# Optimization experiments

Hardware: AMD Instinct MI355X
Metric: run time of the kernel (lower is better)

## Reference

```python
import jax, jax.numpy as jnp
import numpy as np

EPS = 1e-10
WS = 5  # window_size
PAD = WS // 2


def _conv(x, k, pad_h, pad_w):
    # x: [N,1,H,W], k: [1,1,kh,kw], 'same'-style explicit padding
    return jax.lax.conv_general_dilated(
        x, k, window_strides=(1, 1),
        padding=[(pad_h, pad_h), (pad_w, pad_w)],
        dimension_numbers=("NCHW", "OIHW", "NCHW"))


def setup_inputs() -> dict:
    key = jax.random.key(0)
    B, C, Fr, T = 8, 2, 256, 2048
    spectrogram = jax.random.normal(key, (B, C, Fr, T), dtype=jnp.float32)
    # Gaussian kernel (window_size=5, sigma=1.0)
    c = WS // 2
    coords = jnp.arange(WS, dtype=jnp.float32) - c
    yy, xx = jnp.meshgrid(coords, coords, indexing="ij")
    g = jnp.exp(-(xx ** 2 + yy ** 2) / 2.0)
    gaussian_kernel = (g / g.sum()).reshape(1, 1, WS, WS)
    # Sobel kernels / 8
    sobel_x = (jnp.array([[-1, 0, 1], [-2, 0, 2], [-1, 0, 1]], jnp.float32) / 8.0).reshape(1, 1, 3, 3)
    sobel_y = (jnp.array([[-1, -2, -1], [0, 0, 0], [1, 2, 1]], jnp.float32) / 8.0).reshape(1, 1, 3, 3)
    # Harmonic kernel: 7x1 [-1,0,0,2,0,0,-1]
    hk = jnp.zeros(7, jnp.float32).at[0].set(-1.0).at[3].set(2.0).at[6].set(-1.0)
    harmonic_kernel = hk.reshape(1, 1, 7, 1)
    return {"spectrogram": spectrogram, "gaussian_kernel": gaussian_kernel,
            "sobel_x": sobel_x, "sobel_y": sobel_y, "harmonic_kernel": harmonic_kernel}


def _forward(spectrogram, gaussian_kernel, sobel_x, sobel_y, harmonic_kernel):
    B, C, Fr, T = spectrogram.shape
    # Per-channel 1-in/1-out convs == fold channels into batch.
    x = spectrogram.reshape(B * C, 1, Fr, T)

    grad_freq = _conv(x, sobel_y, 1, 1)
    grad_time = _conv(x, sobel_x, 1, 1)
    magnitude = jnp.sqrt(grad_freq ** 2 + grad_time ** 2 + EPS)
    angle = jnp.arctan2(grad_freq, grad_time + EPS)

    # ---- entropy (structure-tensor eigenvalue entropy) ----
    vx = magnitude * jnp.cos(angle)
    vy = magnitude * jnp.sin(angle)
    vxx = _conv(vx * vx, gaussian_kernel, PAD, PAD)
    vyy = _conv(vy * vy, gaussian_kernel, PAD, PAD)
    vxy = _conv(vx * vy, gaussian_kernel, PAD, PAD)
    trace = vxx + vyy
    det = vxx * vyy - vxy * vxy
    disc = jnp.sqrt(jnp.maximum(trace * trace - 4.0 * det, 0.0) + EPS)
    l1 = jnp.maximum((trace + disc) / 2.0, EPS)
    l2 = jnp.maximum((trace - disc) / 2.0, EPS)
    s = l1 + l2 + EPS
    p1, p2 = l1 / s, l2 / s
    entropy = -(p1 * jnp.log(p1 + EPS) + p2 * jnp.log(p2 + EPS)) / np.log(2.0)
    entropy = jnp.clip(entropy, 0.0, 1.0)

    # ---- alignment ----
    ux = jnp.cos(angle)
    uy = jnp.sin(angle)
    ux_avg = _conv(ux, gaussian_kernel, PAD, PAD)
    uy_avg = _conv(uy, gaussian_kernel, PAD, PAD)
    alignment = jnp.clip(jnp.sqrt(ux_avg ** 2 + uy_avg ** 2 + EPS), 0.0, 1.0)

    # ---- curvature ----
    dudx = _conv(ux, sobel_x, 1, 1)
    dudy = _conv(ux, sobel_y, 1, 1)
    dvdx = _conv(uy, sobel_x, 1, 1)
    dvdy = _conv(uy, sobel_y, 1, 1)
    curv = jnp.sqrt(dudx ** 2 + dudy ** 2 + dvdx ** 2 + dvdy ** 2 + EPS)
    curvature = _conv(curv, gaussian_kernel, PAD, PAD)

    # ---- harmonic coherence ----
    harm = jnp.abs(_conv(x, harmonic_kernel, 3, 0))
    local_energy = _conv(x ** 2, gaussian_kernel, PAD, PAD)
    harmonic = jnp.clip(harm / (local_energy + EPS), 0.0, 1.0)

    # ---- temporal stability: inverse temporal gradient magnitude, smoothed ----
    temporal = _conv(1.0 / (1.0 + jnp.abs(grad_time)), gaussian_kernel, PAD, PAD)
    temporal = jnp.clip(temporal, 0.0, 1.0)

    # ---- spectral flow: smoothed frequency-gradient magnitude ----
    spectral = jnp.clip(_conv(jnp.abs(grad_freq), gaussian_kernel, PAD, PAD), 0.0, 1.0)

    def chan_mean(f):  # [B*C,1,F,T] -> [B,1,F,T]
        return f.reshape(B, C, Fr, T).mean(axis=1, keepdims=True)

    return (chan_mean(entropy), chan_mean(alignment), chan_mean(curvature),
            chan_mean(harmonic), chan_mean(temporal), chan_mean(spectral))


def reference(spectrogram, gaussian_kernel, sobel_x, sobel_y, harmonic_kernel):
    return _forward(spectrogram, gaussian_kernel, sobel_x, sobel_y, harmonic_kernel)
```

## Files before the change

### kernel.cpp

```cpp
#include <hip/hip_runtime.h>
#include <hip/hip_fp16.h>


#define F_DIM 256
#define T_DIM 2048
#define B_DIM 8
#define C_DIM 2
#define TILE  32

#define XROWS 40
#define XS    42
#define UROWS 38
#define US    38
#define FROWS 36
#define FS    36
#define FH2   18
#define EPSF  1e-10f

static __device__ __forceinline__ __half2 pack_h2(float a, float b) {
    auto v = __builtin_amdgcn_cvt_pkrtz(a, b);
    return *(__half2*)&v;
}
static __device__ __forceinline__ float clamp01(float x) {
    return fminf(fmaxf(x, 0.f), 1.f);
}

__global__ __launch_bounds__(256, 4)
void audio_struct_fused(const float* __restrict__ x_in,
                        const float* __restrict__ gk_in,
                        float* __restrict__ out)
{
    __shared__ __align__(16) float   s_x [XROWS*XS];
    __shared__ __align__(16) __half2 s_u [UROWS*US];
    __shared__ __align__(16) __half2 s_P0[FROWS*FS];
    __shared__ __align__(16) __half2 s_P1[FROWS*FS];
    __shared__ __align__(16) __half2 s_P2[FROWS*FS];
    __shared__ __align__(16) float   s_tmp[TILE*FS];

    const int tx  = threadIdx.x;
    const int ty  = threadIdx.y;
    const int tid = ty * 32 + tx;
    const int t0  = blockIdx.x * TILE;
    const int f0  = blockIdx.y * TILE;
    const int b   = blockIdx.z;

    float r0 = gk_in[10], r1 = gk_in[11], r2 = gk_in[12], r3 = gk_in[13], r4 = gk_in[14];
    float winv = __builtin_amdgcn_rcpf(r0 + r1 + r2 + r3 + r4);
    const float w[5] = {r0*winv, r1*winv, r2*winv, r3*winv, r4*winv};
    const __half2 wh2[5] = {pack_h2(w[0],w[0]), pack_h2(w[1],w[1]), pack_h2(w[2],w[2]),
                            pack_h2(w[3],w[3]), pack_h2(w[4],w[4])};

    auto vpass_pair = [&](const __half2* src, __half2* dst) {
        const uint2* s = (const uint2*)src;
        uint2* d = (uint2*)dst;
        for (int idx = tid; idx < TILE * FH2; idx += 256) {
            __half2 a0 = pack_h2(0.f, 0.f), a1 = a0;
            #pragma unroll
            for (int i = 0; i < 5; ++i) {
                uint2 v = s[idx + i * FH2];
                a0 = __hfma2(wh2[i], *(const __half2*)&v.x, a0);
                a1 = __hfma2(wh2[i], *(const __half2*)&v.y, a1);
            }
            uint2 o; o.x = *(const unsigned*)&a0; o.y = *(const unsigned*)&a1;
            d[idx] = o;
        }
    };

    float acc[6][4];
    #pragma unroll
    for (int k = 0; k < 6; ++k)
        #pragma unroll
        for (int s = 0; s < 4; ++s) acc[k][s] = 0.0f;

    for (int c = 0; c < C_DIM; ++c) {
        __syncthreads();

        const float* xp = x_in + (size_t)(b * C_DIM + c) * F_DIM * T_DIM;
        for (int idx = tid; idx < XROWS * 20; idx += 256) {
            int r  = idx / 20, c2 = idx % 20;
            int gf = f0 + r - 4;
            int gt = t0 + c2 * 2 - 4;
            float2 v = make_float2(0.f, 0.f);
            if ((unsigned)gf < (unsigned)F_DIM && (unsigned)gt < (unsigned)T_DIM)
                v = *(const float2*)(xp + (size_t)gf * T_DIM + gt);
            *(float2*)&s_x[r * XS + c2 * 2] = v;
        }
        __syncthreads();

        for (int idx = tid; idx < UROWS * UROWS; idx += 256) {
            int r = idx / UROWS, cc = idx % UROWS;
            int gfr = f0 + r - 3, gtc = t0 + cc - 3;
            float ux = 0.f, uy = 0.f, trp = 0.f, dfp = 0.f, sxy = 0.f,
                  tin = 0.f, sf = 0.f;
            if ((unsigned)gfr < (unsigned)F_DIM && (unsigned)gtc < (unsigned)T_DIM) {
                const float* xc = &s_x[(r + 1) * XS + (cc + 1)];
                float x00 = xc[-XS-1], x01 = xc[-XS], x02 = xc[-XS+1];
                float x10 = xc[-1],                   x12 = xc[1];
                float x20 = xc[XS-1],  x21 = xc[XS],  x22 = xc[XS+1];
                float gfv = ((x20 + 2.f*x21 + x22) - (x00 + 2.f*x01 + x02)) * 0.125f;
                float gtv = ((x02 + 2.f*x12 + x22) - (x00 + 2.f*x10 + x20)) * 0.125f;
                float gte = gtv + EPSF;
                float rh  = __builtin_amdgcn_rsqf(gfv * gfv + gte * gte);
                ux = gte * rh;
                uy = gfv * rh;
                float mag = __builtin_amdgcn_sqrtf(gfv * gfv + gtv * gtv + EPSF);
                float vx = mag * ux, vy = mag * uy;
                trp = vx * vx + vy * vy;
                dfp = (vx - vy) * (vx + vy);
                sxy = vx * vy;
                tin = __builtin_amdgcn_rcpf(1.0f + fabsf(gtv));
                sf  = fabsf(gfv);
            }
            s_u[r * US + cc] = pack_h2(ux, uy);
            if (r >= 1 && r < UROWS - 1 && cc >= 1 && cc < UROWS - 1) {
                int fi = (r - 1) * FS + (cc - 1);
                s_P0[fi] = pack_h2(trp, dfp);
                s_P1[fi] = pack_h2(sxy, tin);
                s_P2[fi] = pack_h2(sf, 0.f);
            }
        }
        __syncthreads();

        for (int idx = tid; idx < FROWS * FROWS; idx += 256) {
            int r = idx / FROWS, cc = idx % FROWS;
            int gfr = f0 + r - 2, gtc = t0 + cc - 2;
            float cv = 0.0f;
            if ((unsigned)gfr < (unsigned)F_DIM && (unsigned)gtc < (unsigned)T_DIM) {
                const __half2* up = &s_u[r * US + cc];
                float2 u00 = __half22float2(up[0]),      u01 = __half22float2(up[1]),       u02 = __half22float2(up[2]);
                float2 u10 = __half22float2(up[US]),                                        u12 = __half22float2(up[US+2]);
                float2 u20 = __half22float2(up[2*US]),   u21 = __half22float2(up[2*US+1]),  u22 = __half22float2(up[2*US+2]);
                float dudx = ((u02.x + 2.f*u12.x + u22.x) - (u00.x + 2.f*u10.x + u20.x)) * 0.125f;
                float dudy = ((u20.x + 2.f*u21.x + u22.x) - (u00.x + 2.f*u01.x + u02.x)) * 0.125f;
                float dvdx = ((u02.y + 2.f*u12.y + u22.y) - (u00.y + 2.f*u10.y + u20.y)) * 0.125f;
                float dvdy = ((u20.y + 2.f*u21.y + u22.y) - (u00.y + 2.f*u01.y + u02.y)) * 0.125f;
                cv = __builtin_amdgcn_sqrtf(dudx*dudx + dudy*dudy + dvdx*dvdx + dvdy*dvdy + EPSF);
            }
            ((__half*)s_P2)[2 * (r * FS + cc) + 1] = __float2half_rn(cv);
        }
        __syncthreads();

        float trace_s[4], diff_s[4];
        __half2* tmp_h2 = (__half2*)s_tmp;

        vpass_pair(s_P0, tmp_h2);
        __syncthreads();

        #pragma unroll
        for (int s = 0; s < 4; ++s) {
            int ry = ty + 8 * s;
            float a = 0.f, bv = 0.f;
            #pragma unroll
            for (int j = 0; j < 5; ++j) {
                float2 v = __half22float2(tmp_h2[ry * FS + tx + j]);
                a += w[j] * v.x; bv += w[j] * v.y;
            }
            trace_s[s] = a; diff_s[s] = bv;
        }
        vpass_pair(s_P1, s_P0);
        __syncthreads();

        #pragma unroll
        for (int s = 0; s < 4; ++s) {
            int ry = ty + 8 * s;
            __half2 a = pack_h2(0.f, 0.f);
            #pragma unroll
            for (int j = 0; j < 5; ++j)
                a = __hfma2(wh2[j], s_P0[ry * FS + tx + j], a);
            float2 v = __half22float2(a);
            float trace = trace_s[s], diff = diff_s[s];
            float disc  = __builtin_amdgcn_sqrtf(
                              fmaxf(diff * diff + 4.f * v.x * v.x, 0.f) + EPSF);
            float l1 = fmaxf(0.5f * (trace + disc), EPSF);
            float l2 = fmaxf(0.5f * (trace - disc), EPSF);
            float inv = __builtin_amdgcn_rcpf(l1 + l2 + EPSF);
            float p1 = l1 * inv, p2 = l2 * inv;
            float ent = -(p1 * __builtin_amdgcn_logf(p1 + EPSF)
                        + p2 * __builtin_amdgcn_logf(p2 + EPSF));
            acc[0][s] += 0.5f * clamp01(ent);
            acc[4][s] += 0.5f * clamp01(v.y);
        }
        vpass_pair(s_P2, tmp_h2);
        __syncthreads();

        #pragma unroll
        for (int s = 0; s < 4; ++s) {
            int ry = ty + 8 * s;
            __half2 a = pack_h2(0.f, 0.f);
            #pragma unroll
            for (int j = 0; j < 5; ++j)
                a = __hfma2(wh2[j], tmp_h2[ry * FS + tx + j], a);
            float2 v = __half22float2(a);
            acc[5][s] += 0.5f * clamp01(v.x);
            acc[2][s] += 0.5f * v.y;
        }
        for (int idx = tid; idx < TILE * FS; idx += 256) {
            int r = idx / FS, cc = idx % FS;
            __half2 a = pack_h2(0.f, 0.f);
            #pragma unroll
            for (int i = 0; i < 5; ++i)
                a = __hfma2(wh2[i], s_u[(r + i + 1) * US + (cc + 1)], a);
            s_P1[idx] = a;
        }
        __syncthreads();

        #pragma unroll
        for (int s = 0; s < 4; ++s) {
            int ry = ty + 8 * s;
            __half2 a = pack_h2(0.f, 0.f);
            #pragma unroll
            for (int j = 0; j < 5; ++j)
                a = __hfma2(wh2[j], s_P1[ry * FS + tx + j], a);
            float2 v = __half22float2(a);
            acc[1][s] += 0.5f * clamp01(
                __builtin_amdgcn_sqrtf(v.x * v.x + v.y * v.y + EPSF));
        }
        for (int idx = tid; idx < TILE * FS; idx += 256) {
            int r = idx / FS, cc = idx % FS;
            float a = 0.f;
            #pragma unroll
            for (int i = 0; i < 5; ++i) {
                float xv = s_x[(r + i + 2) * XS + (cc + 2)];
                a += w[i] * xv * xv;
            }
            s_tmp[idx] = a;
        }
        __syncthreads();

        #pragma unroll
        for (int s = 0; s < 4; ++s) {
            int ry = ty + 8 * s;
            float le = 0.f;
            #pragma unroll
            for (int j = 0; j < 5; ++j)
                le += w[j] * s_tmp[ry * FS + tx + j];
            float xm  = s_x[(ry + 1) * XS + tx + 4];
            float x0v = s_x[(ry + 4) * XS + tx + 4];
            float xpv = s_x[(ry + 7) * XS + tx + 4];
            float harm = fabsf(2.f * x0v - xm - xpv);
            acc[3][s] += 0.5f * clamp01(harm * __builtin_amdgcn_rcpf(le + EPSF));
        }
    }

    const size_t plane = (size_t)B_DIM * F_DIM * T_DIM;
    const size_t base  = (size_t)b * F_DIM * T_DIM + (size_t)f0 * T_DIM + t0 + tx;
    #pragma unroll
    for (int k = 0; k < 6; ++k)
        #pragma unroll
        for (int s = 0; s < 4; ++s)
            out[k * plane + base + (size_t)(ty + 8 * s) * T_DIM] = acc[k][s];
}

extern "C" void kernel_launch(void* const* d_in, const int* in_sizes, int n_in,
                              void* d_out, int out_size, void* d_ws, size_t ws_size,
                              hipStream_t stream) {
    const float* x  = (const float*)d_in[0];
    const float* gk = (const float*)d_in[1];
    float* out = (float*)d_out;
    dim3 grid(T_DIM / TILE, F_DIM / TILE, B_DIM);
    dim3 block(32, 8);
    audio_struct_fused<<<grid, block, 0, stream>>>(x, gk, out);
}
```

Measured before the change: 226.5 us.

## Specialize interior tiles, vectorize smem vertical passes, compute curvature Sobel in half2

Adds a compile-time interior path that drops bounds checks on global loads and on the stage-A and stage-B masks for tiles away from the borders. Shared-memory pitches change so the vertical passes over s_u and s_x can use 8-byte vector loads that handle two columns at once. The curvature Sobel now runs in packed half2 arithmetic, and the structure-tensor products are rewritten algebraically so the explicit magnitude and vx/vy products are gone. In exchange, computing the gradients in half precision loses accuracy, and the extra template instantiation makes the kernel larger.

Measured after the change: 222.5 us. No clear change (-1.8%).

```diff
diff --git a/kernel.cpp b/kernel.cpp
--- a/kernel.cpp
+++ b/kernel.cpp
@@ -9,13 +9,15 @@
 #define TILE  32
 
 #define XROWS 40
-#define XS    42
+#define XS    40
 #define UROWS 38
-#define US    38
+#define US    40
 #define FROWS 36
 #define FS    36
 #define FH2   18
 #define EPSF  1e-10f
+
+template<bool V> struct BoolC { static constexpr bool value = V; };
 
 static __device__ __forceinline__ __half2 pack_h2(float a, float b) {
     auto v = __builtin_amdgcn_cvt_pkrtz(a, b);
@@ -49,12 +51,15 @@
     const float w[5] = {r0*winv, r1*winv, r2*winv, r3*winv, r4*winv};
     const __half2 wh2[5] = {pack_h2(w[0],w[0]), pack_h2(w[1],w[1]), pack_h2(w[2],w[2]),
                             pack_h2(w[3],w[3]), pack_h2(w[4],w[4])};
+    const __half2 h2z    = pack_h2(0.f, 0.f);
+    const __half2 two    = pack_h2(2.f, 2.f);
+    const __half2 eighth = pack_h2(0.125f, 0.125f);
 
     auto vpass_pair = [&](const __half2* src, __half2* dst) {
         const uint2* s = (const uint2*)src;
         uint2* d = (uint2*)dst;
         for (int idx = tid; idx < TILE * FH2; idx += 256) {
-            __half2 a0 = pack_h2(0.f, 0.f), a1 = a0;
+            __half2 a0 = h2z, a1 = h2z;
             #pragma unroll
             for (int i = 0; i < 5; ++i) {
                 uint2 v = s[idx + i * FH2];
@@ -72,27 +77,38 @@
         #pragma unroll
         for (int s = 0; s < 4; ++s) acc[k][s] = 0.0f;
 
-    for (int c = 0; c < C_DIM; ++c) {
-        __syncthreads();
-
-        const float* xp = x_in + (size_t)(b * C_DIM + c) * F_DIM * T_DIM;
+    const bool interior = (f0 >= 4) && (f0 + TILE + 4 <= F_DIM) &&
+                          (t0 >= 4) && (t0 + TILE + 4 <= T_DIM);
+
+    auto phaseABC = [&](const float* xp, auto FASTC) {
+        constexpr bool FAST = decltype(FASTC)::value;
+
         for (int idx = tid; idx < XROWS * 20; idx += 256) {
-            int r  = idx / 20, c2 = idx % 20;
-            int gf = f0 + r - 4;
-            int gt = t0 + c2 * 2 - 4;
-            float2 v = make_float2(0.f, 0.f);
-            if ((unsigned)gf < (unsigned)F_DIM && (unsigned)gt < (unsigned)T_DIM)
-                v = *(const float2*)(xp + (size_t)gf * T_DIM + gt);
+            int r  = idx / 20, c2 = idx - r * 20;
+            float2 v;
+            if (FAST) {
+                v = *(const float2*)(xp + (size_t)(f0 + r - 4) * T_DIM + (t0 + c2 * 2 - 4));
+            } else {
+                int gf = f0 + r - 4;
+                int gt = t0 + c2 * 2 - 4;
+                v = make_float2(0.f, 0.f);
+                if ((unsigned)gf < (unsigned)F_DIM && (unsigned)gt < (unsigned)T_DIM)
+                    v = *(const float2*)(xp + (size_t)gf * T_DIM + gt);
+            }
             *(float2*)&s_x[r * XS + c2 * 2] = v;
         }
         __syncthreads();
 
         for (int idx = tid; idx < UROWS * UROWS; idx += 256) {
-            int r = idx / UROWS, cc = idx % UROWS;
-            int gfr = f0 + r - 3, gtc = t0 + cc - 3;
+            int r = idx / UROWS, cc = idx - r * UROWS;
             float ux = 0.f, uy = 0.f, trp = 0.f, dfp = 0.f, sxy = 0.f,
                   tin = 0.f, sf = 0.f;
-            if ((unsigned)gfr < (unsigned)F_DIM && (unsigned)gtc < (unsigned)T_DIM) {
+            bool ok = true;
+            if (!FAST) {
+                int gfr = f0 + r - 3, gtc = t0 + cc - 3;
+                ok = ((unsigned)gfr < (unsigned)F_DIM) & ((unsigned)gtc < (unsigned)T_DIM);
+            }
+            if (ok) {
                 const float* xc = &s_x[(r + 1) * XS + (cc + 1)];
                 float x00 = xc[-XS-1], x01 = xc[-XS], x02 = xc[-XS+1];
                 float x10 = xc[-1],                   x12 = xc[1];
@@ -100,18 +116,19 @@
                 float gfv = ((x20 + 2.f*x21 + x22) - (x00 + 2.f*x01 + x02)) * 0.125f;
                 float gtv = ((x02 + 2.f*x12 + x22) - (x00 + 2.f*x10 + x20)) * 0.125f;
                 float gte = gtv + EPSF;
-                float rh  = __builtin_amdgcn_rsqf(gfv * gfv + gte * gte);
+                float g2f = gfv * gfv;
+                float d2  = fmaf(gte, gte, g2f);
+                float rh  = __builtin_amdgcn_rsqf(d2);
                 ux = gte * rh;
                 uy = gfv * rh;
-                float mag = __builtin_amdgcn_sqrtf(gfv * gfv + gtv * gtv + EPSF);
-                float vx = mag * ux, vy = mag * uy;
-                trp = vx * vx + vy * vy;
-                dfp = (vx - vy) * (vx + vy);
-                sxy = vx * vy;
+                float m2 = fmaf(gtv, gtv, g2f) + EPSF;
+                trp = m2;
+                dfp = m2 * (ux - uy) * (ux + uy);
+                sxy = m2 * ux * uy;
                 tin = __builtin_amdgcn_rcpf(1.0f + fabsf(gtv));
                 sf  = fabsf(gfv);
             }
-            s_u[r * US + cc] = pack_h2(ux, uy);
+            s_u[r * US + cc + 1] = pack_h2(ux, uy);
             if (r >= 1 && r < UROWS - 1 && cc >= 1 && cc < UROWS - 1) {
                 int fi = (r - 1) * FS + (cc - 1);
                 s_P0[fi] = pack_h2(trp, dfp);
@@ -122,23 +139,38 @@
         __syncthreads();
 
         for (int idx = tid; idx < FROWS * FROWS; idx += 256) {
-            int r = idx / FROWS, cc = idx % FROWS;
-            int gfr = f0 + r - 2, gtc = t0 + cc - 2;
-            float cv = 0.0f;
-            if ((unsigned)gfr < (unsigned)F_DIM && (unsigned)gtc < (unsigned)T_DIM) {
-                const __half2* up = &s_u[r * US + cc];
-                float2 u00 = __half22float2(up[0]),      u01 = __half22float2(up[1]),       u02 = __half22float2(up[2]);
-                float2 u10 = __half22float2(up[US]),                                        u12 = __half22float2(up[US+2]);
-                float2 u20 = __half22float2(up[2*US]),   u21 = __half22float2(up[2*US+1]),  u22 = __half22float2(up[2*US+2]);
-                float dudx = ((u02.x + 2.f*u12.x + u22.x) - (u00.x + 2.f*u10.x + u20.x)) * 0.125f;
-                float dudy = ((u20.x + 2.f*u21.x + u22.x) - (u00.x + 2.f*u01.x + u02.x)) * 0.125f;
-                float dvdx = ((u02.y + 2.f*u12.y + u22.y) - (u00.y + 2.f*u10.y + u20.y)) * 0.125f;
-                float dvdy = ((u20.y + 2.f*u21.y + u22.y) - (u00.y + 2.f*u01.y + u02.y)) * 0.125f;
-                cv = __builtin_amdgcn_sqrtf(dudx*dudx + dudy*dudy + dvdx*dvdx + dvdy*dvdy + EPSF);
+            int r = idx / FROWS, cc = idx - r * FROWS;
+            const __half2* up = &s_u[r * US + cc + 1];
+            __half2 u00 = up[0],      u01 = up[1],      u02 = up[2];
+            __half2 u10 = up[US],                       u12 = up[US+2];
+            __half2 u20 = up[2*US],   u21 = up[2*US+1], u22 = up[2*US+2];
+            __half2 l0 = __hadd2(u00, u20); l0 = __hfma2(two, u10, l0);
+            __half2 l2 = __hadd2(u02, u22); l2 = __hfma2(two, u12, l2);
+            __half2 dxv = __hmul2(__hsub2(l2, l0), eighth);
+            __half2 t0h = __hadd2(u00, u02); t0h = __hfma2(two, u01, t0h);
+            __half2 t2h = __hadd2(u20, u22); t2h = __hfma2(two, u21, t2h);
+            __half2 dyv = __hmul2(__hsub2(t2h, t0h), eighth);
+            float2 fx = __half22float2(dxv);
+            float2 fy = __half22float2(dyv);
+            float cv = __builtin_amdgcn_sqrtf(
+                fmaf(fx.x, fx.x, fmaf(fx.y, fx.y,
+                fmaf(fy.x, fy.x, fy.y * fy.y))) + EPSF);
+            if (!FAST) {
+                int gfr = f0 + r - 2, gtc = t0 + cc - 2;
+                if (!(((unsigned)gfr < (unsigned)F_DIM) &
+                      ((unsigned)gtc < (unsigned)T_DIM))) cv = 0.f;
             }
             ((__half*)s_P2)[2 * (r * FS + cc) + 1] = __float2half_rn(cv);
         }
         __syncthreads();
+    };
+
+    for (int c = 0; c < C_DIM; ++c) {
+        __syncthreads();
+
+        const float* xp = x_in + (size_t)(b * C_DIM + c) * F_DIM * T_DIM;
+        if (interior) phaseABC(xp, BoolC<true>{});
+        else          phaseABC(xp, BoolC<false>{});
 
         float trace_s[4], diff_s[4];
         __half2* tmp_h2 = (__half2*)s_tmp;
@@ -163,7 +195,7 @@
         #pragma unroll
         for (int s = 0; s < 4; ++s) {
             int ry = ty + 8 * s;
-            __half2 a = pack_h2(0.f, 0.f);
+            __half2 a = h2z;
             #pragma unroll
             for (int j = 0; j < 5; ++j)
                 a = __hfma2(wh2[j], s_P0[ry * FS + tx + j], a);
@@ -186,7 +218,7 @@
         #pragma unroll
         for (int s = 0; s < 4; ++s) {
             int ry = ty + 8 * s;
-            __half2 a = pack_h2(0.f, 0.f);
+            __half2 a = h2z;
             #pragma unroll
             for (int j = 0; j < 5; ++j)
                 a = __hfma2(wh2[j], tmp_h2[ry * FS + tx + j], a);
@@ -194,20 +226,29 @@
             acc[5][s] += 0.5f * clamp01(v.x);
             acc[2][s] += 0.5f * v.y;
         }
-        for (int idx = tid; idx < TILE * FS; idx += 256) {
-            int r = idx / FS, cc = idx % FS;
-            __half2 a = pack_h2(0.f, 0.f);
-            #pragma unroll
-            for (int i = 0; i < 5; ++i)
-                a = __hfma2(wh2[i], s_u[(r + i + 1) * US + (cc + 1)], a);
-            s_P1[idx] = a;
-        }
-        __syncthreads();
-
-        #pragma unroll
-        for (int s = 0; s < 4; ++s) {
-            int ry = ty + 8 * s;
-            __half2 a = pack_h2(0.f, 0.f);
+        {
+            const uint2* su2 = (const uint2*)s_u;
+            uint2* dP1 = (uint2*)s_P1;
+            for (int idx = tid; idx < TILE * FH2; idx += 256) {
+                int r = idx / FH2, p = idx - r * FH2;
+                const uint2* sp = su2 + (r + 1) * (US/2) + 1 + p;
+                __half2 a0 = h2z, a1 = h2z;
+                #pragma unroll
+                for (int i = 0; i < 5; ++i) {
+                    uint2 v = sp[i * (US/2)];
+                    a0 = __hfma2(wh2[i], *(const __half2*)&v.x, a0);
+                    a1 = __hfma2(wh2[i], *(const __half2*)&v.y, a1);
+                }
+                uint2 o; o.x = *(const unsigned*)&a0; o.y = *(const unsigned*)&a1;
+                dP1[idx] = o;
+            }
+        }
+        __syncthreads();
+
+        #pragma unroll
+        for (int s = 0; s < 4; ++s) {
+            int ry = ty + 8 * s;
+            __half2 a = h2z;
             #pragma unroll
             for (int j = 0; j < 5; ++j)
                 a = __hfma2(wh2[j], s_P1[ry * FS + tx + j], a);
@@ -215,15 +256,21 @@
             acc[1][s] += 0.5f * clamp01(
                 __builtin_amdgcn_sqrtf(v.x * v.x + v.y * v.y + EPSF));
         }
-        for (int idx = tid; idx < TILE * FS; idx += 256) {
-            int r = idx / FS, cc = idx % FS;
-            float a = 0.f;
-            #pragma unroll
-            for (int i = 0; i < 5; ++i) {
-                float xv = s_x[(r + i + 2) * XS + (cc + 2)];
-                a += w[i] * xv * xv;
-            }
-            s_tmp[idx] = a;
+        {
+            const float2* sx2 = (const float2*)s_x;
+            float2* dt2 = (float2*)s_tmp;
+            for (int idx = tid; idx < TILE * FH2; idx += 256) {
+                int r = idx / FH2, p = idx - r * FH2;
+                const float2* sp = sx2 + (r + 2) * (XS/2) + 1 + p;
+                float a = 0.f, bv = 0.f;
+                #pragma unroll
+                for (int i = 0; i < 5; ++i) {
+                    float2 v = sp[i * (XS/2)];
+                    a  = fmaf(w[i], v.x * v.x, a);
+                    bv = fmaf(w[i], v.y * v.y, bv);
+                }
+                dt2[idx] = make_float2(a, bv);
+            }
         }
         __syncthreads();
 
```
